# Kernel optimization log

Hardware: AMD Instinct MI355X
Metric: run time of the kernel (lower is better)

## Reference

```python
import jax, jax.numpy as jnp
import numpy as np

NEG_SLOPE = 0.01  # LeakyReLU default
STRIDE = 5        # group_length // 4
EPS = 1e-5        # RMSNorm eps


def leaky_relu(x):
    return jnp.where(x >= 0, x, NEG_SLOPE * x)


def rmsnorm(x, w):
    return x * jax.lax.rsqrt(jnp.mean(x * x, axis=-1, keepdims=True) + EPS) * w


def s6(x, fc1_w, fc1_b, fc2_w, fc2_b, fc3_w, fc3_b, A):
    # x: [B, L, D] with D = 2*d_model; A: [D, N]
    delta = jax.nn.softplus(x @ fc1_w.T + fc1_b)        # [B, L, D]
    Bm = x @ fc2_w.T + fc2_b                             # [B, L, N]
    Cm = x @ fc3_w.T + fc3_b                             # [B, L, N]
    dA = jnp.exp(jnp.einsum('bld,dn->bldn', delta, A))   # [B, L, D, N]
    dBx = jnp.einsum('bld,bln,bld->bldn', delta, Bm, x)  # delta * B * x

    def step(h, inp):
        dA_t, dBx_t = inp
        h = dA_t * h + dBx_t
        return h, h

    B_, L, D, N = dA.shape
    h0 = jnp.zeros((B_, D, N), dtype=x.dtype)
    _, hs = jax.lax.scan(step, h0, (jnp.swapaxes(dA, 0, 1), jnp.swapaxes(dBx, 0, 1)))
    hs = jnp.swapaxes(hs, 0, 1)                          # [B, L, D, N]
    return jnp.einsum('bln,bldn->bld', Cm, hs)           # [B, L, D]


def setup_inputs() -> dict:
    key = jax.random.key(0)
    ks = iter(jax.random.split(key, 32))

    def rn(shape, scale=0.02):
        return scale * jax.random.normal(next(ks), shape, dtype=jnp.float32)

    B, band, gl, d, N, L = 256, 189, 20, 128, 128, 34
    di = 2 * d
    return {
        'x': jax.random.normal(next(ks), (B, 1, band), dtype=jnp.float32),
        'conv_w': rn((d, 1, gl)), 'conv_b': rn((d,)),
        'norm_w': jnp.ones((d,), jnp.float32),
        'inp_w': rn((di, d)), 'inp_b': rn((di,)),
        'seqconv_w': rn((L, L, 3)), 'seqconv_b': rn((L,)),
        'convlin_w': rn((di, di)), 'convlin_b': rn((di,)),
        'fc1_w': rn((di, di)), 'fc1_b': rn((di,)),
        'fc2_w': rn((N, di)), 'fc2_b': rn((N,)),
        'fc3_w': rn((N, di)), 'fc3_b': rn((N,)),
        'A': jnp.ones((di, N), jnp.float32) / jnp.sqrt(jnp.float32(N)),
        'D_w': rn((di, d)), 'D_b': rn((di,)),
        'out_w': rn((d, di)), 'out_b': rn((d,)),
        'fnn1_w': rn((64, L * d)), 'fnn1_b': rn((64,)),
        'fnn2_w': rn((32, 64)), 'fnn2_b': rn((32,)),
    }


def reference(x, conv_w, conv_b, norm_w, inp_w, inp_b, seqconv_w, seqconv_b,
              convlin_w, convlin_b, fc1_w, fc1_b, fc2_w, fc2_b, fc3_w, fc3_b,
              A, D_w, D_b, out_w, out_b, fnn1_w, fnn1_b, fnn2_w, fnn2_b):
    # group division: Conv1d(1, d, k=20, stride=5) + LeakyReLU
    g = jax.lax.conv_general_dilated(x, conv_w, (STRIDE,), [(0, 0)],
                                     dimension_numbers=('NCH', 'OIH', 'NCH'))
    g = leaky_relu(g + conv_b[None, :, None])            # [B, d, L]
    h = jnp.swapaxes(g, 1, 2)                            # [B, L, d]
    # Mamba block
    xn = rmsnorm(h, norm_w)
    xp = xn @ inp_w.T + inp_b                            # [B, L, 2d]
    # Conv1d(seq_len, seq_len, k=3, pad=1): seq axis L is the channel dim
    xc = jax.lax.conv_general_dilated(xp, seqconv_w, (1,), [(1, 1)],
                                      dimension_numbers=('NCH', 'OIH', 'NCH'))
    xc = jax.nn.silu(xc + seqconv_b[None, :, None])
    xc = xc @ convlin_w.T + convlin_b                    # [B, L, 2d]
    xs = s6(xc, fc1_w, fc1_b, fc2_w, fc2_b, fc3_w, fc3_b, A)
    y = jax.nn.silu(xs) * jax.nn.silu(xn @ D_w.T + D_b)  # gated
    y = y @ out_w.T + out_b                              # [B, L, d]
    # FNN head
    f = y.reshape(y.shape[0], -1)                        # [B, L*d]
    f = leaky_relu(f @ fnn1_w.T + fnn1_b)
    return f @ fnn2_w.T + fnn2_b                         # [B, 32]
```

## Files before the change

kernel.cpp:

```cpp
#include <hip/hip_runtime.h>
#include <math.h>


#define NB    256
#define LL    34
#define DD    128
#define DI    256
#define NN    128
#define MM    (NB*LL)

using u16 = unsigned short;
typedef __attribute__((ext_vector_type(8))) short short8;
typedef __attribute__((ext_vector_type(4))) float f32x4;

__device__ __forceinline__ float silu_f(float x)  { return x / (1.f + __expf(-x)); }
__device__ __forceinline__ float softplus_f(float x) {
    return fmaxf(x, 0.f) + __logf(1.f + __expf(-fabsf(x)));
}
__device__ __forceinline__ float leaky_f(float x) { return (x >= 0.f) ? x : 0.01f * x; }

__device__ __forceinline__ u16 f2bf(float x) {
    unsigned u = __float_as_uint(x);
    return (u16)((u + 0x7FFF + ((u >> 16) & 1)) >> 16);
}
__device__ __forceinline__ float bf2f(u16 h) {
    return __uint_as_float(((unsigned)h) << 16);
}
__device__ __forceinline__ void f2pair(float v, u16* h, u16* l) {
    u16 hh = f2bf(v);
    *h = hh;
    *l = f2bf(v - bf2f(hh));
}

__global__ __launch_bounds__(256)
void prep_conv_k(const float* __restrict__ x, const float* __restrict__ cw,
                 const float* __restrict__ cb, const float* __restrict__ nw,
                 u16* __restrict__ XNh, u16* __restrict__ XNl,
                 const float* __restrict__ inp_w, const float* __restrict__ D_w,
                 const float* __restrict__ fc1_w, const float* __restrict__ fc2_w,
                 const float* __restrict__ fc3_w, const float* __restrict__ convlin_w,
                 const float* __restrict__ out_w,
                 const float* __restrict__ inp_b, const float* __restrict__ D_b,
                 const float* __restrict__ fc1_b, const float* __restrict__ fc2_b,
                 const float* __restrict__ fc3_b,
                 const float* __restrict__ W1, const float* __restrict__ A,
                 u16* __restrict__ wc1h, u16* __restrict__ wc1l,
                 u16* __restrict__ wc3h, u16* __restrict__ wc3l,
                 u16* __restrict__ cvh,  u16* __restrict__ cvl,
                 u16* __restrict__ owh,  u16* __restrict__ owl,
                 float* __restrict__ bias1, float* __restrict__ bias3,
                 float* __restrict__ W1T, int* __restrict__ flag)
{
    const int bx  = blockIdx.x;
    const int tid = threadIdx.x;
    __shared__ float tile[64][65];
    __shared__ float wsum[4];

    if (bx < 4352) {
        const int row = tid >> 7;
        const int c   = tid & 127;
        const int bl  = bx * 2 + row;
        const int b   = bl / LL, l = bl % LL;
        const float* xr = x + (size_t)b * 189 + l * 5;
        float g = cb[c];
        #pragma unroll
        for (int k = 0; k < 20; k++) g = fmaf(xr[k], cw[c * 20 + k], g);
        g = leaky_f(g);

        float s = g * g;
        #pragma unroll
        for (int m = 32; m >= 1; m >>= 1) s += __shfl_xor(s, m);
        if ((tid & 63) == 0) wsum[tid >> 6] = s;
        __syncthreads();
        float mean = (wsum[row * 2] + wsum[row * 2 + 1]) * (1.f / 128.f);
        float inv = 1.f / sqrtf(mean + 1e-5f);
        float v = g * inv * nw[c];
        f2pair(v, &XNh[(size_t)bl * DD + c], &XNl[(size_t)bl * DD + c]);
    } else if (bx < 5504) {
        int i = (bx - 4352) * 256 + tid;
        if (i < 65536) {
            float v = (i < 32768) ? inp_w[i] : D_w[i - 32768];
            f2pair(v, &wc1h[i], &wc1l[i]);
        } else if (i < 196608) {
            int j = i - 65536;
            float v = (j < 65536) ? fc1_w[j] : (j < 98304 ? fc2_w[j - 65536] : fc3_w[j - 98304]);
            f2pair(v, &wc3h[j], &wc3l[j]);
        } else if (i < 262144) {
            int j = i - 196608;
            f2pair(convlin_w[j], &cvh[j], &cvl[j]);
        } else if (i < 294912) {
            int j = i - 262144;
            f2pair(out_w[j], &owh[j], &owl[j]);
        }
        if (i < 512)  bias1[i] = (i < 256) ? inp_b[i] : D_b[i - 256];
        else if (i < 1024) {
            int j = i - 512;
            bias3[j] = (j < 256) ? fc1_b[j] : (j < 384 ? fc2_b[j - 256] : fc3_b[j - 384]);
        }
    } else if (bx < 5572) {
        const int bt = bx - 5504;
        for (int p = 0; p < 16; p++) {
            int idx = tid + p * 256;
            int r = idx >> 6, c = idx & 63;
            tile[r][c] = W1[(size_t)r * 4352 + bt * 64 + c];
        }
        __syncthreads();
        for (int p = 0; p < 16; p++) {
            int idx = tid + p * 256;
            int cc = idx >> 6, rr = idx & 63;
            W1T[(size_t)(bt * 64 + cc) * 64 + rr] = tile[rr][cc];
        }
    } else {
        __shared__ int s;
        if (tid == 0) s = 1;
        __syncthreads();
        bool ok = true;
        for (int k = 0; k < 128; k++) {
            int idx = tid + k * 256;
            ok &= (A[idx] == A[idx & ~127]);
        }
        if (!ok) s = 0;
        __syncthreads();
        if (tid == 0) *flag = s;
    }
}

template <int K, int EPI>
__global__ __launch_bounds__(256)
void mgemm_k(const u16* __restrict__ Ah, const u16* __restrict__ Al,
             const u16* __restrict__ Wh, const u16* __restrict__ Wl,
             const float* __restrict__ bias,
             float* __restrict__ Y, int ldy,
             u16* __restrict__ Yh, u16* __restrict__ Yl,
             u16* __restrict__ BC)
{
    const int tid  = threadIdx.x;
    const int r0   = blockIdx.x * 128;
    const int c0   = blockIdx.y * 64;
    const int wave = tid >> 6;
    const int lane = tid & 63;
    const int wm   = wave & 1;
    const int wn   = wave >> 1;
    const int l15  = lane & 15;
    const int lq   = lane >> 4;

    __shared__ u16 sAh[128][40];
    __shared__ u16 sAl[128][40];
    __shared__ u16 sBh[64][40];
    __shared__ u16 sBl[64][40];

    f32x4 acc[4][2];
    #pragma unroll
    for (int i = 0; i < 4; i++)
        #pragma unroll
        for (int j = 0; j < 2; j++) acc[i][j] = (f32x4){0.f, 0.f, 0.f, 0.f};

    const int a_row = tid >> 1;
    const int a_kb  = (tid & 1) * 16;
    const int b_row = tid >> 2;
    const int b_ko  = (tid & 3) * 8;

    for (int k0 = 0; k0 < K; k0 += 32) {
        const u16* ga = Ah + (size_t)(r0 + a_row) * K + k0 + a_kb;
        const u16* gl = Al + (size_t)(r0 + a_row) * K + k0 + a_kb;
        short8 vh0 = *(const short8*)(ga);
        short8 vh1 = *(const short8*)(ga + 8);
        short8 vl0 = *(const short8*)(gl);
        short8 vl1 = *(const short8*)(gl + 8);
        const u16* gb = Wh + (size_t)(c0 + b_row) * K + k0 + b_ko;
        const u16* gc = Wl + (size_t)(c0 + b_row) * K + k0 + b_ko;
        short8 wb = *(const short8*)(gb);
        short8 wc = *(const short8*)(gc);

        *(short8*)&sAh[a_row][a_kb]     = vh0;
        *(short8*)&sAh[a_row][a_kb + 8] = vh1;
        *(short8*)&sAl[a_row][a_kb]     = vl0;
        *(short8*)&sAl[a_row][a_kb + 8] = vl1;
        *(short8*)&sBh[b_row][b_ko] = wb;
        *(short8*)&sBl[b_row][b_ko] = wc;
        __syncthreads();

        short8 fah[4], fal[4], fbh[2], fbl[2];
        #pragma unroll
        for (int i = 0; i < 4; i++) {
            fah[i] = *(const short8*)&sAh[wm * 64 + i * 16 + l15][lq * 8];
            fal[i] = *(const short8*)&sAl[wm * 64 + i * 16 + l15][lq * 8];
        }
        #pragma unroll
        for (int j = 0; j < 2; j++) {
            fbh[j] = *(const short8*)&sBh[wn * 32 + j * 16 + l15][lq * 8];
            fbl[j] = *(const short8*)&sBl[wn * 32 + j * 16 + l15][lq * 8];
        }
        #pragma unroll
        for (int i = 0; i < 4; i++)
            #pragma unroll
            for (int j = 0; j < 2; j++) {
                acc[i][j] = __builtin_amdgcn_mfma_f32_16x16x32_bf16(fah[i], fbh[j], acc[i][j], 0, 0, 0);
                acc[i][j] = __builtin_amdgcn_mfma_f32_16x16x32_bf16(fah[i], fbl[j], acc[i][j], 0, 0, 0);
                acc[i][j] = __builtin_amdgcn_mfma_f32_16x16x32_bf16(fal[i], fbh[j], acc[i][j], 0, 0, 0);
            }
        __syncthreads();
    }

    #pragma unroll
    for (int i = 0; i < 4; i++) {
        int gr = r0 + wm * 64 + i * 16 + lq * 4;
        #pragma unroll
        for (int j = 0; j < 2; j++) {
            int gc = c0 + wn * 32 + j * 16 + l15;
            float bb = bias[gc];
            #pragma unroll
            for (int r = 0; r < 4; r++) {
                float v = acc[i][j][r] + bb;
                if (EPI == 1 || EPI == 3) { if (gc < 256) v = softplus_f(v); }
                if (EPI == 2) {
                    u16 hh, ll;
                    f2pair(v, &hh, &ll);
                    Yh[(size_t)(gr + r) * ldy + gc] = hh;
                    Yl[(size_t)(gr + r) * ldy + gc] = ll;
                } else {
                    Y[(size_t)(gr + r) * ldy + gc] = v;
                    if (EPI == 3 && gc >= 256) {
                        u16 hh, ll;
                        f2pair(v, &hh, &ll);
                        u16* rb = BC + (size_t)(gr + r) * 1024
                                     + ((gc < 384) ? 0 : 256) + (gc & 127);
                        rb[0]   = hh;
                        rb[128] = ll;
                    }
                }
            }
        }
    }
}

__global__ __launch_bounds__(1024, 1)
void mega2_k(const int* __restrict__ flag,
             const float* __restrict__ buf1,
             const float* __restrict__ scw, const float* __restrict__ scb,
             const u16* __restrict__ cvh, const u16* __restrict__ cvl,
             const float* __restrict__ clb,
             const u16* __restrict__ wc3h, const u16* __restrict__ wc3l,
             const float* __restrict__ bias3,
             const float* __restrict__ A,
             const u16* __restrict__ owh, const u16* __restrict__ owl,
             const float* __restrict__ outb,
             float* __restrict__ buf3,
             u16* __restrict__ bcpair,
             u16* __restrict__ xc2h, u16* __restrict__ xc2l,
             float* __restrict__ fout)
{
    const int b    = blockIdx.x;
    const int tid  = threadIdx.x;
    const int wave = tid >> 6;
    const int lane = tid & 63;
    const int l15  = lane & 15;
    const int lq   = lane >> 4;

    __shared__ __align__(16) char smem[109584];
    float (*sx)[264] = (float (*)[264])(smem);
    float (*sw)[112] = (float (*)[112])(smem + 35904);
    u16 (*sXch)[264] = (u16 (*)[264])(smem);
    u16 (*sXcl)[264] = (u16 (*)[264])(smem + 25344);
    u16 (*sBh)[136]  = (u16 (*)[136])(smem);
    u16 (*sBl)[136]  = (u16 (*)[136])(smem + 13056);
    u16 (*sCh)[136]  = (u16 (*)[136])(smem + 26112);
    u16 (*sCl)[136]  = (u16 (*)[136])(smem + 39168);
    u16 (*sGh)[264]  = (u16 (*)[264])(smem);
    u16 (*sGl)[264]  = (u16 (*)[264])(smem + 25344);
    u16 (*sX2h)[264] = (u16 (*)[264])(smem + 52224);
    u16 (*sX2l)[264] = (u16 (*)[264])(smem + 77568);
    float (*sM)[49]  = (float (*)[49])(smem + 102912);

    const bool uni = (*flag != 0);

    for (int idx = tid; idx < LL * 256; idx += 1024) {
        int li = idx >> 8, jj = idx & 255;
        sx[li][jj + 1] = buf1[(size_t)(b * LL + li) * 512 + jj];
    }
    if (tid < LL) { sx[tid][0] = 0.f; sx[tid][257] = 0.f; }
    for (int idx = tid; idx < LL * LL * 3; idx += 1024) {
        int lo = idx / 102;
        int rem = idx - lo * 102;
        int li = rem / 3;
        int k  = rem - li * 3;
        sw[li][lo * 3 + k] = scw[idx];
    }
    __syncthreads();

    {
        const int tx  = tid & 63;
        const int ty  = tid >> 6;
        const int j0c = tx * 4;
        const int cbase = (ty < 2) ? ty * 3 : 6 + (ty - 2) * 2;
        const int ccnt  = (ty < 2) ? 3 : 2;

        float cacc[3][4];
        #pragma unroll
        for (int i = 0; i < 3; i++)
            #pragma unroll
            for (int jj = 0; jj < 4; jj++) cacc[i][jj] = 0.f;

        for (int li = 0; li < LL; li++) {
            float4 xa = *(const float4*)&sx[li][j0c];
            float2 xb = *(const float2*)&sx[li][j0c + 4];
            float xv[6] = {xa.x, xa.y, xa.z, xa.w, xb.x, xb.y};
            const float* swr = &sw[li][0];
            #pragma unroll
            for (int i = 0; i < 3; i++) {
                if (i < ccnt) {
                    int lo3 = (cbase + i) * 3;
                    float w0 = swr[lo3 + 0];
                    float w1 = swr[lo3 + 1];
                    float w2 = swr[lo3 + 2];
                    #pragma unroll
                    for (int jj = 0; jj < 4; jj++) {
                        cacc[i][jj] = fmaf(w0, xv[jj],     cacc[i][jj]);
                        cacc[i][jj] = fmaf(w1, xv[jj + 1], cacc[i][jj]);
                        cacc[i][jj] = fmaf(w2, xv[jj + 2], cacc[i][jj]);
                    }
                }
            }
        }
        __syncthreads();

        #pragma unroll
        for (int i = 0; i < 3; i++) {
            if (i < ccnt) {
                int lo = cbase + i;
                float bb = scb[lo];
                ushort4 oh, ol;
                float v0 = silu_f(cacc[i][0] + bb);
                float v1 = silu_f(cacc[i][1] + bb);
                float v2 = silu_f(cacc[i][2] + bb);
                float v3 = silu_f(cacc[i][3] + bb);
                f2pair(v0, &oh.x, &ol.x);
                f2pair(v1, &oh.y, &ol.y);
                f2pair(v2, &oh.z, &ol.z);
                f2pair(v3, &oh.w, &ol.w);
                *(ushort4*)&sXch[lo][j0c] = oh;
                *(ushort4*)&sXcl[lo][j0c] = ol;
            }
        }
    }
    __syncthreads();

    {
        const int c0 = wave * 16;
        f32x4 a2[3];
        #pragma unroll
        for (int i = 0; i < 3; i++) a2[i] = (f32x4){0.f, 0.f, 0.f, 0.f};

        #pragma unroll
        for (int ks = 0; ks < 8; ks++) {
            short8 fh[3], fl[3];
            #pragma unroll
            for (int i = 0; i < 3; i++) {
                fh[i] = *(const short8*)&sXch[i * 16 + l15][ks * 32 + lq * 8];
                fl[i] = *(const short8*)&sXcl[i * 16 + l15][ks * 32 + lq * 8];
            }
            const size_t wo = (size_t)(c0 + l15) * 256 + ks * 32 + lq * 8;
            short8 bh = *(const short8*)&cvh[wo];
            short8 bl = *(const short8*)&cvl[wo];
            #pragma unroll
            for (int i = 0; i < 3; i++) {
                a2[i] = __builtin_amdgcn_mfma_f32_16x16x32_bf16(fh[i], bh, a2[i], 0, 0, 0);
                a2[i] = __builtin_amdgcn_mfma_f32_16x16x32_bf16(fh[i], bl, a2[i], 0, 0, 0);
                a2[i] = __builtin_amdgcn_mfma_f32_16x16x32_bf16(fl[i], bh, a2[i], 0, 0, 0);
            }
        }
        #pragma unroll
        for (int i = 0; i < 3; i++) {
            int row = i * 16 + lq * 4;
            int col = c0 + l15;
            float bb = clb[col];
            #pragma unroll
            for (int r = 0; r < 4; r++) {
                float v = a2[i][r] + bb;
                u16 hh, ll;
                f2pair(v, &hh, &ll);
                sX2h[row + r][col] = hh;
                sX2l[row + r][col] = ll;
                if (!uni && (row + r) < LL) {
                    xc2h[(size_t)(b * LL + row + r) * 256 + col] = hh;
                    xc2l[(size_t)(b * LL + row + r) * 256 + col] = ll;
                }
            }
        }
    }
    __syncthreads();

    {
        const int c0 = wave * 32;
        f32x4 a3[3][2];
        #pragma unroll
        for (int i = 0; i < 3; i++)
            #pragma unroll
            for (int j = 0; j < 2; j++) a3[i][j] = (f32x4){0.f, 0.f, 0.f, 0.f};

        #pragma unroll
        for (int ks = 0; ks < 8; ks++) {
            short8 fh[3], fl[3];
            #pragma unroll
            for (int i = 0; i < 3; i++) {
                fh[i] = *(const short8*)&sX2h[i * 16 + l15][ks * 32 + lq * 8];
                fl[i] = *(const short8*)&sX2l[i * 16 + l15][ks * 32 + lq * 8];
            }
            #pragma unroll
            for (int j = 0; j < 2; j++) {
                const size_t wo = (size_t)(c0 + j * 16 + l15) * 256 + ks * 32 + lq * 8;
                short8 bh = *(const short8*)&wc3h[wo];
                short8 bl = *(const short8*)&wc3l[wo];
                #pragma unroll
                for (int i = 0; i < 3; i++) {
                    a3[i][j] = __builtin_amdgcn_mfma_f32_16x16x32_bf16(fh[i], bh, a3[i][j], 0, 0, 0);
                    a3[i][j] = __builtin_amdgcn_mfma_f32_16x16x32_bf16(fh[i], bl, a3[i][j], 0, 0, 0);
                    a3[i][j] = __builtin_amdgcn_mfma_f32_16x16x32_bf16(fl[i], bh, a3[i][j], 0, 0, 0);
                }
            }
        }
        #pragma unroll
        for (int i = 0; i < 3; i++) {
            int row = i * 16 + lq * 4;
            #pragma unroll
            for (int j = 0; j < 2; j++) {
                int col = c0 + j * 16 + l15;
                float bb = bias3[col];
                #pragma unroll
                for (int r = 0; r < 4; r++) {
                    float v = a3[i][j][r] + bb;
                    int rr = row + r;
                    if (col < 256) {
                        v = softplus_f(v);
                        if (rr < LL) buf3[((size_t)b * LL + rr) * 512 + col] = v;
                    } else {
                        u16 hh, ll;
                        f2pair(v, &hh, &ll);
                        int cc = col & 127;
                        if (col < 384) { sBh[rr][cc] = hh; sBl[rr][cc] = ll; }
                        else           { sCh[rr][cc] = hh; sCl[rr][cc] = ll; }
                        if (!uni && rr < LL) {
                            buf3[((size_t)b * LL + rr) * 512 + col] = v;
                            u16* rb = bcpair + ((size_t)b * LL + rr) * 1024
                                      + ((col < 384) ? 0 : 256) + cc;
                            rb[0]   = hh;
                            rb[128] = ll;
                        }
                    }
                }
            }
        }
    }
    __syncthreads();
    if (!uni) return;

    for (int tt = wave; tt < 9; tt += 16) {
        int ti = tt / 3, tj = tt - ti * 3;
        f32x4 acc = (f32x4){0.f, 0.f, 0.f, 0.f};
        #pragma unroll
        for (int ks = 0; ks < 4; ks++) {
            short8 ch = *(const short8*)&sCh[ti * 16 + l15][ks * 32 + lq * 8];
            short8 cl = *(const short8*)&sCl[ti * 16 + l15][ks * 32 + lq * 8];
            short8 bh = *(const short8*)&sBh[tj * 16 + l15][ks * 32 + lq * 8];
            short8 bl = *(const short8*)&sBl[tj * 16 + l15][ks * 32 + lq * 8];
            acc = __builtin_amdgcn_mfma_f32_16x16x32_bf16(ch, bh, acc, 0, 0, 0);
            acc = __builtin_amdgcn_mfma_f32_16x16x32_bf16(ch, bl, acc, 0, 0, 0);
            acc = __builtin_amdgcn_mfma_f32_16x16x32_bf16(cl, bh, acc, 0, 0, 0);
        }
        #pragma unroll
        for (int r = 0; r < 4; r++) {
            int row = ti * 16 + lq * 4 + r;
            if (row < LL) sM[row][tj * 16 + l15] = acc[r];
        }
    }
    __syncthreads();

    if (tid < 256) {
        const int d = tid;
        const float a_d = A[(size_t)d * NN];
        const float* pDel = buf3 + (size_t)b * LL * 512 + d;

        float u[LL], eS[LL];
        float S = 0.f;
        #pragma unroll
        for (int l = 0; l < LL; l++) {
            float dl = pDel[l * 512];
            S = fmaf(dl, a_d, S);
            eS[l] = __expf(S);
            float xv = bf2f(sX2h[l][d]) + bf2f(sX2l[l][d]);
            u[l] = __expf(-S) * dl * xv;
        }

        const float* pG = buf1 + (size_t)b * LL * 512 + 256 + d;
        #pragma unroll
        for (int l = 0; l < LL; l++) {
            float acc = 0.f;
            for (int t = 0; t <= l; t++) acc = fmaf(sM[l][t], u[t], acc);
            float xs = eS[l] * acc;
            float g = silu_f(xs) * silu_f(pG[l * 512]);
            u16 hh, ll2;
            f2pair(g, &hh, &ll2);
            sGh[l][d] = hh;
            sGl[l][d] = ll2;
        }
    } else {
        u16* zh = &sGh[34][0];
        u16* zl = &sGl[34][0];
        for (int idx = tid - 256; idx < 14 * 264; idx += 768) {
            zh[idx] = 0;
            zl[idx] = 0;
        }
    }
    __syncthreads();

    {
        const int j0 = wave & 7;
        const int i0 = (wave >> 3) ? 2 : 0;
        const int ni = (wave >> 3) ? 1 : 2;
        f32x4 a4[2];
        #pragma unroll
        for (int i = 0; i < 2; i++) a4[i] = (f32x4){0.f, 0.f, 0.f, 0.f};
        #pragma unroll
        for (int ks = 0; ks < 8; ks++) {
            const size_t wo = (size_t)(j0 * 16 + l15) * 256 + ks * 32 + lq * 8;
            short8 bh = *(const short8*)&owh[wo];
            short8 bl = *(const short8*)&owl[wo];
            #pragma unroll
            for (int i = 0; i < 2; i++) {
                if (i < ni) {
                    short8 ah = *(const short8*)&sGh[(i0 + i) * 16 + l15][ks * 32 + lq * 8];
                    short8 al = *(const short8*)&sGl[(i0 + i) * 16 + l15][ks * 32 + lq * 8];
                    a4[i] = __builtin_amdgcn_mfma_f32_16x16x32_bf16(ah, bh, a4[i], 0, 0, 0);
                    a4[i] = __builtin_amdgcn_mfma_f32_16x16x32_bf16(ah, bl, a4[i], 0, 0, 0);
                    a4[i] = __builtin_amdgcn_mfma_f32_16x16x32_bf16(al, bh, a4[i], 0, 0, 0);
                }
            }
        }
        #pragma unroll
        for (int i = 0; i < 2; i++) {
            if (i < ni) {
                int row = (i0 + i) * 16 + lq * 4;
                int col = j0 * 16 + l15;
                float bb = outb[col];
                #pragma unroll
                for (int r = 0; r < 4; r++)
                    if (row + r < LL)
                        fout[(size_t)(b * LL + row + r) * 128 + col] = a4[i][r] + bb;
            }
        }
    }
}

__global__ __launch_bounds__(256)
void scan_fb_k(const int* __restrict__ flag,
               const float* __restrict__ dBC,
               const u16*  __restrict__ Xh, const u16* __restrict__ Xl,
               const float* __restrict__ A,
               const float* __restrict__ DG,
               u16* __restrict__ Gh, u16* __restrict__ Gl)
{
    if (*flag != 0) return;
    const int b  = blockIdx.y;
    const int d0 = blockIdx.x * 64;
    const int tid = threadIdx.x;
    const int sub = tid & 15;
    const int pg  = tid >> 4;
    const int dbase = d0 + pg * 4;
    const int nA = sub * 4;

    float a[4][8], h[4][8];
    #pragma unroll
    for (int dd = 0; dd < 4; dd++) {
        const float* Ar = A + (size_t)(dbase + dd) * NN;
        float4 q0 = *(const float4*)(Ar + nA);
        float4 q1 = *(const float4*)(Ar + 64 + nA);
        a[dd][0]=q0.x; a[dd][1]=q0.y; a[dd][2]=q0.z; a[dd][3]=q0.w;
        a[dd][4]=q1.x; a[dd][5]=q1.y; a[dd][6]=q1.z; a[dd][7]=q1.w;
        #pragma unroll
        for (int j = 0; j < 8; j++) h[dd][j] = 0.f;
    }

    const float* pD  = dBC + (size_t)b * LL * 512 + dbase;
    const float* pBC = dBC + (size_t)b * LL * 512 + 256 + nA;
    const u16*  pXh = Xh  + (size_t)b * LL * 256 + dbase;
    const u16*  pXl = Xl  + (size_t)b * LL * 256 + dbase;
    const float* pG  = DG  + (size_t)b * LL * 512 + 256 + dbase;
    u16* pGh = Gh + (size_t)b * LL * 256 + dbase;
    u16* pGl = Gl + (size_t)b * LL * 256 + dbase;

    for (int l = 0; l < LL; l++) {
        float4  cD  = *(const float4*)(pD);
        ushort4 cXh = *(const ushort4*)(pXh);
        ushort4 cXl = *(const ushort4*)(pXl);
        float4 cB0 = *(const float4*)(pBC);
        float4 cB1 = *(const float4*)(pBC + 64);
        float4 cC0 = *(const float4*)(pBC + 128);
        float4 cC1 = *(const float4*)(pBC + 192);
        pD += 512; pBC += 512; pXh += 256; pXl += 256;

        float xv[4] = { bf2f(cXh.x) + bf2f(cXl.x), bf2f(cXh.y) + bf2f(cXl.y),
                        bf2f(cXh.z) + bf2f(cXl.z), bf2f(cXh.w) + bf2f(cXl.w) };
        float dl[4] = {cD.x, cD.y, cD.z, cD.w};
        float dx[4] = {cD.x * xv[0], cD.y * xv[1], cD.z * xv[2], cD.w * xv[3]};
        float bv[8] = {cB0.x,cB0.y,cB0.z,cB0.w,cB1.x,cB1.y,cB1.z,cB1.w};
        float cv[8] = {cC0.x,cC0.y,cC0.z,cC0.w,cC1.x,cC1.y,cC1.z,cC1.w};

        float accd[4] = {0.f, 0.f, 0.f, 0.f};
        #pragma unroll
        for (int dd = 0; dd < 4; dd++)
            #pragma unroll
            for (int j = 0; j < 8; j++) {
                float dA = __expf(dl[dd] * a[dd][j]);
                h[dd][j] = fmaf(dA, h[dd][j], dx[dd] * bv[j]);
                accd[dd] = fmaf(cv[j], h[dd][j], accd[dd]);
            }
        #pragma unroll
        for (int dd = 0; dd < 4; dd++) {
            float v = accd[dd];
            v += __shfl_xor(v, 1);
            v += __shfl_xor(v, 2);
            v += __shfl_xor(v, 4);
            v += __shfl_xor(v, 8);
            accd[dd] = v;
        }
        if (sub == 0) {
            float4 dg = *(const float4*)(pG);
            ushort4 oh, ol;
            float g0 = silu_f(accd[0]) * silu_f(dg.x);
            float g1 = silu_f(accd[1]) * silu_f(dg.y);
            float g2 = silu_f(accd[2]) * silu_f(dg.z);
            float g3 = silu_f(accd[3]) * silu_f(dg.w);
            f2pair(g0, &oh.x, &ol.x);
            f2pair(g1, &oh.y, &ol.y);
            f2pair(g2, &oh.z, &ol.z);
            f2pair(g3, &oh.w, &ol.w);
            *(ushort4*)pGh = oh;
            *(ushort4*)pGl = ol;
        }
        pG += 512; pGh += 256; pGl += 256;
    }
}

__global__ __launch_bounds__(512)
void tail_cold_k(const int* __restrict__ flag,
                 const u16* __restrict__ gFh, const u16* __restrict__ gFl,
                 const u16* __restrict__ owh, const u16* __restrict__ owl,
                 const float* __restrict__ outb,
                 float* __restrict__ fout)
{
    if (*flag != 0) return;
    const int b    = blockIdx.x;
    const int tid  = threadIdx.x;
    const int wave = tid >> 6;
    const int lane = tid & 63;
    const int l15  = lane & 15;
    const int lq   = lane >> 4;

    __shared__ u16 sGh[48][264];
    __shared__ u16 sGl[48][264];

    for (int idx = tid; idx < LL * 32; idx += 512) {
        int l = idx >> 5, c = (idx & 31) << 3;
        *(short8*)&sGh[l][c] = *(const short8*)&gFh[((size_t)b * LL + l) * 256 + c];
        *(short8*)&sGl[l][c] = *(const short8*)&gFl[((size_t)b * LL + l) * 256 + c];
    }
    {
        u16* zh = &sGh[34][0];
        u16* zl = &sGl[34][0];
        for (int idx = tid; idx < 14 * 264; idx += 512) {
            zh[idx] = 0;
            zl[idx] = 0;
        }
    }
    __syncthreads();

    const int j0 = wave;
    f32x4 a4[3];
    #pragma unroll
    for (int i = 0; i < 3; i++) a4[i] = (f32x4){0.f, 0.f, 0.f, 0.f};
    #pragma unroll
    for (int ks = 0; ks < 8; ks++) {
        const size_t wo = (size_t)(j0 * 16 + l15) * 256 + ks * 32 + lq * 8;
        short8 bh = *(const short8*)&owh[wo];
        short8 bl = *(const short8*)&owl[wo];
        #pragma unroll
        for (int i = 0; i < 3; i++) {
            short8 ah = *(const short8*)&sGh[i * 16 + l15][ks * 32 + lq * 8];
            short8 al = *(const short8*)&sGl[i * 16 + l15][ks * 32 + lq * 8];
            a4[i] = __builtin_amdgcn_mfma_f32_16x16x32_bf16(ah, bh, a4[i], 0, 0, 0);
            a4[i] = __builtin_amdgcn_mfma_f32_16x16x32_bf16(ah, bl, a4[i], 0, 0, 0);
            a4[i] = __builtin_amdgcn_mfma_f32_16x16x32_bf16(al, bh, a4[i], 0, 0, 0);
        }
    }
    #pragma unroll
    for (int i = 0; i < 3; i++) {
        int row = i * 16 + lq * 4;
        int col = j0 * 16 + l15;
        float bb = outb[col];
        #pragma unroll
        for (int r = 0; r < 4; r++)
            if (row + r < LL)
                fout[(size_t)(b * LL + row + r) * 128 + col] = a4[i][r] + bb;
    }
}

__global__ __launch_bounds__(256)
void fnn1_k(const float* __restrict__ F, const float* __restrict__ W1T,
            float* __restrict__ partials)
{
    const int btile = blockIdx.x;
    const int kc    = blockIdx.y;
    const int tid   = threadIdx.x;
    __shared__ float sf[16][260];
    for (int i = tid; i < 16 * 256; i += 256) {
        int r = i >> 8, c = i & 255;
        sf[r][c] = F[(size_t)(btile * 16 + r) * 4352 + kc * 256 + c];
    }
    __syncthreads();

    const int o  = tid & 63;
    const int bq = tid >> 6;
    const float* w = W1T + (size_t)(kc * 256) * 64 + o;
    float acc[4] = {0.f, 0.f, 0.f, 0.f};
    for (int k = 0; k < 256; k += 4) {
        float w0 = w[(size_t)(k + 0) * 64];
        float w1 = w[(size_t)(k + 1) * 64];
        float w2 = w[(size_t)(k + 2) * 64];
        float w3 = w[(size_t)(k + 3) * 64];
        #pragma unroll
        for (int bj = 0; bj < 4; bj++) {
            float4 f4 = *(const float4*)&sf[bq * 4 + bj][k];
            acc[bj] = fmaf(w0, f4.x, acc[bj]);
            acc[bj] = fmaf(w1, f4.y, acc[bj]);
            acc[bj] = fmaf(w2, f4.z, acc[bj]);
            acc[bj] = fmaf(w3, f4.w, acc[bj]);
        }
    }
    #pragma unroll
    for (int bj = 0; bj < 4; bj++)
        partials[(size_t)kc * 16384 + (btile * 16 + bq * 4 + bj) * 64 + o] = acc[bj];
}

__global__ __launch_bounds__(64)
void fnn2_k(const float* __restrict__ partials,
            const float* __restrict__ B1,
            const float* __restrict__ W2, const float* __restrict__ B2,
            float* __restrict__ out)
{
    int b = blockIdx.x;
    int t = threadIdx.x;
    __shared__ float s1[64];
    float acc = B1[t];
    #pragma unroll
    for (int kc = 0; kc < 17; kc++)
        acc += partials[(size_t)kc * 16384 + b * 64 + t];
    s1[t] = leaky_f(acc);
    __syncthreads();

    if (t < 32) {
        float acc2 = B2[t];
        const float* w2 = W2 + t * 64;
        #pragma unroll
        for (int j = 0; j < 64; j++) acc2 = fmaf(s1[j], w2[j], acc2);
        out[(size_t)b * 32 + t] = acc2;
    }
}

extern "C" void kernel_launch(void* const* d_in, const int* in_sizes, int n_in,
                              void* d_out, int out_size, void* d_ws, size_t ws_size,
                              hipStream_t stream)
{
    const float* x        = (const float*)d_in[0];
    const float* conv_w   = (const float*)d_in[1];
    const float* conv_b   = (const float*)d_in[2];
    const float* norm_w   = (const float*)d_in[3];
    const float* inp_w    = (const float*)d_in[4];
    const float* inp_b    = (const float*)d_in[5];
    const float* seqconv_w= (const float*)d_in[6];
    const float* seqconv_b= (const float*)d_in[7];
    const float* convlin_w= (const float*)d_in[8];
    const float* convlin_b= (const float*)d_in[9];
    const float* fc1_w    = (const float*)d_in[10];
    const float* fc1_b    = (const float*)d_in[11];
    const float* fc2_w    = (const float*)d_in[12];
    const float* fc2_b    = (const float*)d_in[13];
    const float* fc3_w    = (const float*)d_in[14];
    const float* fc3_b    = (const float*)d_in[15];
    const float* A        = (const float*)d_in[16];
    const float* D_w      = (const float*)d_in[17];
    const float* D_b      = (const float*)d_in[18];
    const float* out_w    = (const float*)d_in[19];
    const float* out_b    = (const float*)d_in[20];
    const float* fnn1_w   = (const float*)d_in[21];
    const float* fnn1_b   = (const float*)d_in[22];
    const float* fnn2_w   = (const float*)d_in[23];
    const float* fnn2_b   = (const float*)d_in[24];

    char* W = (char*)d_ws;
    float* buf1  = (float*)(W + 0);
    float* buf3  = (float*)(W + 17825792);
    u16*   xnh   = (u16*)  (W + 35651584);
    u16*   xnl   = (u16*)  (W + 37879808);
    u16*   xc2h  = (u16*)  (W + 35651584);
    float* fout  = (float*)(W + 35651584);
    u16*   xc2l  = (u16*)  (W + 40108032);
    u16*   gateh = (u16*)  (W + 44564480);
    u16*   gatel = (u16*)  (W + 49020928);
    float* w1t   = (float*)(W + 53477376);
    u16*   wc1h  = (u16*)  (W + 54591488);
    u16*   wc1l  = (u16*)  (W + 54722560);
    u16*   wc3h  = (u16*)  (W + 54853632);
    u16*   wc3l  = (u16*)  (W + 55115776);
    u16*   cvh   = (u16*)  (W + 55377920);
    u16*   cvl   = (u16*)  (W + 55508992);
    u16*   owh   = (u16*)  (W + 55640064);
    u16*   owl   = (u16*)  (W + 55705600);
    float* bias1 = (float*)(W + 55771136);
    float* bias3 = (float*)(W + 55773184);
    int*   uflag = (int*)  (W + 55775232);
    u16* bcpair = (u16*)buf1;
    float* partials = buf3;

    prep_conv_k<<<5573, 256, 0, stream>>>(x, conv_w, conv_b, norm_w, xnh, xnl,
                                          inp_w, D_w, fc1_w, fc2_w, fc3_w,
                                          convlin_w, out_w,
                                          inp_b, D_b, fc1_b, fc2_b, fc3_b,
                                          fnn1_w, A,
                                          wc1h, wc1l, wc3h, wc3l, cvh, cvl,
                                          owh, owl, bias1, bias3, w1t, uflag);

    mgemm_k<128, 0><<<dim3(MM / 128, 8), 256, 0, stream>>>(
        xnh, xnl, wc1h, wc1l, bias1, buf1, 512, nullptr, nullptr, nullptr);

    mega2_k<<<NB, 1024, 0, stream>>>(uflag, buf1, seqconv_w, seqconv_b,
                                     cvh, cvl, convlin_b, wc3h, wc3l, bias3,
                                     A, owh, owl, out_b,
                                     buf3, bcpair, xc2h, xc2l, fout);

    scan_fb_k<<<dim3(4, NB), 256, 0, stream>>>(uflag, buf3, xc2h, xc2l, A,
                                               buf1, gateh, gatel);
    tail_cold_k<<<NB, 512, 0, stream>>>(uflag, gateh, gatel, owh, owl, out_b,
                                        fout);

    fnn1_k<<<dim3(16, 17), 256, 0, stream>>>(fout, w1t, partials);
    fnn2_k<<<NB, 64, 0, stream>>>(partials, fnn1_b, fnn2_w, fnn2_b,
                                  (float*)d_out);
}
```

Measured before the change: 205.5 us.

## Fuse conv+RMSNorm and input projection GEMM into per-batch mega kernel

Moves the strided conv, LeakyReLU and RMSNorm, plus the inp/D projection GEMM, out of the prep kernel and a separate MFMA GEMM launch and into the per-batch mega2 kernel. The normalized activations stay in shared memory. The projected x and the gate values go straight to LDS, so the 17MB buf1 round trip and one kernel launch are removed. In exchange LDS use grows to about 145KB per block. Each 1024-thread block now also redoes the small GEMM with weights read from global memory and not tiled through LDS. The gate is still written to global only in the non-uniform fallback path.

After: 204.8 us. No clear change (-0.3%).

```diff
diff --git a/kernel.cpp b/kernel.cpp
--- a/kernel.cpp
+++ b/kernel.cpp
@@ -33,51 +33,27 @@
 }
 
 __global__ __launch_bounds__(256)
-void prep_conv_k(const float* __restrict__ x, const float* __restrict__ cw,
-                 const float* __restrict__ cb, const float* __restrict__ nw,
-                 u16* __restrict__ XNh, u16* __restrict__ XNl,
-                 const float* __restrict__ inp_w, const float* __restrict__ D_w,
-                 const float* __restrict__ fc1_w, const float* __restrict__ fc2_w,
-                 const float* __restrict__ fc3_w, const float* __restrict__ convlin_w,
-                 const float* __restrict__ out_w,
-                 const float* __restrict__ inp_b, const float* __restrict__ D_b,
-                 const float* __restrict__ fc1_b, const float* __restrict__ fc2_b,
-                 const float* __restrict__ fc3_b,
-                 const float* __restrict__ W1, const float* __restrict__ A,
-                 u16* __restrict__ wc1h, u16* __restrict__ wc1l,
-                 u16* __restrict__ wc3h, u16* __restrict__ wc3l,
-                 u16* __restrict__ cvh,  u16* __restrict__ cvl,
-                 u16* __restrict__ owh,  u16* __restrict__ owl,
-                 float* __restrict__ bias1, float* __restrict__ bias3,
-                 float* __restrict__ W1T, int* __restrict__ flag)
+void prep_k(const float* __restrict__ inp_w, const float* __restrict__ D_w,
+            const float* __restrict__ fc1_w, const float* __restrict__ fc2_w,
+            const float* __restrict__ fc3_w, const float* __restrict__ convlin_w,
+            const float* __restrict__ out_w,
+            const float* __restrict__ inp_b, const float* __restrict__ D_b,
+            const float* __restrict__ fc1_b, const float* __restrict__ fc2_b,
+            const float* __restrict__ fc3_b,
+            const float* __restrict__ W1, const float* __restrict__ A,
+            u16* __restrict__ wc1h, u16* __restrict__ wc1l,
+            u16* __restrict__ wc3h, u16* __restrict__ wc3l,
+            u16* __restrict__ cvh,  u16* __restrict__ cvl,
+            u16* __restrict__ owh,  u16* __restrict__ owl,
+            float* __restrict__ bias1, float* __restrict__ bias3,
+            float* __restrict__ W1T, int* __restrict__ flag)
 {
     const int bx  = blockIdx.x;
     const int tid = threadIdx.x;
     __shared__ float tile[64][65];
-    __shared__ float wsum[4];
-
-    if (bx < 4352) {
-        const int row = tid >> 7;
-        const int c   = tid & 127;
-        const int bl  = bx * 2 + row;
-        const int b   = bl / LL, l = bl % LL;
-        const float* xr = x + (size_t)b * 189 + l * 5;
-        float g = cb[c];
-        #pragma unroll
-        for (int k = 0; k < 20; k++) g = fmaf(xr[k], cw[c * 20 + k], g);
-        g = leaky_f(g);
-
-        float s = g * g;
-        #pragma unroll
-        for (int m = 32; m >= 1; m >>= 1) s += __shfl_xor(s, m);
-        if ((tid & 63) == 0) wsum[tid >> 6] = s;
-        __syncthreads();
-        float mean = (wsum[row * 2] + wsum[row * 2 + 1]) * (1.f / 128.f);
-        float inv = 1.f / sqrtf(mean + 1e-5f);
-        float v = g * inv * nw[c];
-        f2pair(v, &XNh[(size_t)bl * DD + c], &XNl[(size_t)bl * DD + c]);
-    } else if (bx < 5504) {
-        int i = (bx - 4352) * 256 + tid;
+
+    if (bx < 1152) {
+        int i = bx * 256 + tid;
         if (i < 65536) {
             float v = (i < 32768) ? inp_w[i] : D_w[i - 32768];
             f2pair(v, &wc1h[i], &wc1l[i]);
@@ -97,8 +73,8 @@
             int j = i - 512;
             bias3[j] = (j < 256) ? fc1_b[j] : (j < 384 ? fc2_b[j - 256] : fc3_b[j - 384]);
         }
-    } else if (bx < 5572) {
-        const int bt = bx - 5504;
+    } else if (bx < 1220) {
+        const int bt = bx - 1152;
         for (int p = 0; p < 16; p++) {
             int idx = tid + p * 256;
             int r = idx >> 6, c = idx & 63;
@@ -125,118 +101,13 @@
     }
 }
 
-template <int K, int EPI>
-__global__ __launch_bounds__(256)
-void mgemm_k(const u16* __restrict__ Ah, const u16* __restrict__ Al,
-             const u16* __restrict__ Wh, const u16* __restrict__ Wl,
-             const float* __restrict__ bias,
-             float* __restrict__ Y, int ldy,
-             u16* __restrict__ Yh, u16* __restrict__ Yl,
-             u16* __restrict__ BC)
-{
-    const int tid  = threadIdx.x;
-    const int r0   = blockIdx.x * 128;
-    const int c0   = blockIdx.y * 64;
-    const int wave = tid >> 6;
-    const int lane = tid & 63;
-    const int wm   = wave & 1;
-    const int wn   = wave >> 1;
-    const int l15  = lane & 15;
-    const int lq   = lane >> 4;
-
-    __shared__ u16 sAh[128][40];
-    __shared__ u16 sAl[128][40];
-    __shared__ u16 sBh[64][40];
-    __shared__ u16 sBl[64][40];
-
-    f32x4 acc[4][2];
-    #pragma unroll
-    for (int i = 0; i < 4; i++)
-        #pragma unroll
-        for (int j = 0; j < 2; j++) acc[i][j] = (f32x4){0.f, 0.f, 0.f, 0.f};
-
-    const int a_row = tid >> 1;
-    const int a_kb  = (tid & 1) * 16;
-    const int b_row = tid >> 2;
-    const int b_ko  = (tid & 3) * 8;
-
-    for (int k0 = 0; k0 < K; k0 += 32) {
-        const u16* ga = Ah + (size_t)(r0 + a_row) * K + k0 + a_kb;
-        const u16* gl = Al + (size_t)(r0 + a_row) * K + k0 + a_kb;
-        short8 vh0 = *(const short8*)(ga);
-        short8 vh1 = *(const short8*)(ga + 8);
-        short8 vl0 = *(const short8*)(gl);
-        short8 vl1 = *(const short8*)(gl + 8);
-        const u16* gb = Wh + (size_t)(c0 + b_row) * K + k0 + b_ko;
-        const u16* gc = Wl + (size_t)(c0 + b_row) * K + k0 + b_ko;
-        short8 wb = *(const short8*)(gb);
-        short8 wc = *(const short8*)(gc);
-
-        *(short8*)&sAh[a_row][a_kb]     = vh0;
-        *(short8*)&sAh[a_row][a_kb + 8] = vh1;
-        *(short8*)&sAl[a_row][a_kb]     = vl0;
-        *(short8*)&sAl[a_row][a_kb + 8] = vl1;
-        *(short8*)&sBh[b_row][b_ko] = wb;
-        *(short8*)&sBl[b_row][b_ko] = wc;
-        __syncthreads();
-
-        short8 fah[4], fal[4], fbh[2], fbl[2];
-        #pragma unroll
-        for (int i = 0; i < 4; i++) {
-            fah[i] = *(const short8*)&sAh[wm * 64 + i * 16 + l15][lq * 8];
-            fal[i] = *(const short8*)&sAl[wm * 64 + i * 16 + l15][lq * 8];
-        }
-        #pragma unroll
-        for (int j = 0; j < 2; j++) {
-            fbh[j] = *(const short8*)&sBh[wn * 32 + j * 16 + l15][lq * 8];
-            fbl[j] = *(const short8*)&sBl[wn * 32 + j * 16 + l15][lq * 8];
-        }
-        #pragma unroll
-        for (int i = 0; i < 4; i++)
-            #pragma unroll
-            for (int j = 0; j < 2; j++) {
-                acc[i][j] = __builtin_amdgcn_mfma_f32_16x16x32_bf16(fah[i], fbh[j], acc[i][j], 0, 0, 0);
-                acc[i][j] = __builtin_amdgcn_mfma_f32_16x16x32_bf16(fah[i], fbl[j], acc[i][j], 0, 0, 0);
-                acc[i][j] = __builtin_amdgcn_mfma_f32_16x16x32_bf16(fal[i], fbh[j], acc[i][j], 0, 0, 0);
-            }
-        __syncthreads();
-    }
-
-    #pragma unroll
-    for (int i = 0; i < 4; i++) {
-        int gr = r0 + wm * 64 + i * 16 + lq * 4;
-        #pragma unroll
-        for (int j = 0; j < 2; j++) {
-            int gc = c0 + wn * 32 + j * 16 + l15;
-            float bb = bias[gc];
-            #pragma unroll
-            for (int r = 0; r < 4; r++) {
-                float v = acc[i][j][r] + bb;
-                if (EPI == 1 || EPI == 3) { if (gc < 256) v = softplus_f(v); }
-                if (EPI == 2) {
-                    u16 hh, ll;
-                    f2pair(v, &hh, &ll);
-                    Yh[(size_t)(gr + r) * ldy + gc] = hh;
-                    Yl[(size_t)(gr + r) * ldy + gc] = ll;
-                } else {
-                    Y[(size_t)(gr + r) * ldy + gc] = v;
-                    if (EPI == 3 && gc >= 256) {
-                        u16 hh, ll;
-                        f2pair(v, &hh, &ll);
-                        u16* rb = BC + (size_t)(gr + r) * 1024
-                                     + ((gc < 384) ? 0 : 256) + (gc & 127);
-                        rb[0]   = hh;
-                        rb[128] = ll;
-                    }
-                }
-            }
-        }
-    }
-}
-
 __global__ __launch_bounds__(1024, 1)
 void mega2_k(const int* __restrict__ flag,
-             const float* __restrict__ buf1,
+             const float* __restrict__ x,
+             const float* __restrict__ cw, const float* __restrict__ cb,
+             const float* __restrict__ nw,
+             const u16* __restrict__ wc1h, const u16* __restrict__ wc1l,
+             const float* __restrict__ bias1,
              const float* __restrict__ scw, const float* __restrict__ scb,
              const u16* __restrict__ cvh, const u16* __restrict__ cvl,
              const float* __restrict__ clb,
@@ -245,6 +116,7 @@
              const float* __restrict__ A,
              const u16* __restrict__ owh, const u16* __restrict__ owl,
              const float* __restrict__ outb,
+             float* __restrict__ buf1,
              float* __restrict__ buf3,
              u16* __restrict__ bcpair,
              u16* __restrict__ xc2h, u16* __restrict__ xc2l,
@@ -257,7 +129,7 @@
     const int l15  = lane & 15;
     const int lq   = lane >> 4;
 
-    __shared__ __align__(16) char smem[109584];
+    __shared__ __align__(16) char smem[144944];
     float (*sx)[264] = (float (*)[264])(smem);
     float (*sw)[112] = (float (*)[112])(smem + 35904);
     u16 (*sXch)[264] = (u16 (*)[264])(smem);
@@ -268,17 +140,16 @@
     u16 (*sCl)[136]  = (u16 (*)[136])(smem + 39168);
     u16 (*sGh)[264]  = (u16 (*)[264])(smem);
     u16 (*sGl)[264]  = (u16 (*)[264])(smem + 25344);
+    u16 (*sXnh)[136] = (u16 (*)[136])(smem + 52224);
+    u16 (*sXnl)[136] = (u16 (*)[136])(smem + 65280);
     u16 (*sX2h)[264] = (u16 (*)[264])(smem + 52224);
     u16 (*sX2l)[264] = (u16 (*)[264])(smem + 77568);
     float (*sM)[49]  = (float (*)[49])(smem + 102912);
+    float (*sDG)[260]= (float (*)[260])(smem + 109584);
+    __shared__ float wsumP[16];
 
     const bool uni = (*flag != 0);
 
-    for (int idx = tid; idx < LL * 256; idx += 1024) {
-        int li = idx >> 8, jj = idx & 255;
-        sx[li][jj + 1] = buf1[(size_t)(b * LL + li) * 512 + jj];
-    }
-    if (tid < LL) { sx[tid][0] = 0.f; sx[tid][257] = 0.f; }
     for (int idx = tid; idx < LL * LL * 3; idx += 1024) {
         int lo = idx / 102;
         int rem = idx - lo * 102;
@@ -286,6 +157,89 @@
         int k  = rem - li * 3;
         sw[li][lo * 3 + k] = scw[idx];
     }
+
+    {
+        const int rp = tid >> 7;
+        const int c  = tid & 127;
+        for (int pass = 0; pass < 5; pass++) {
+            const int rr = pass * 8 + rp;
+            float g = 0.f, s = 0.f;
+            if (rr < LL) {
+                const float* xr = x + (size_t)b * 189 + rr * 5;
+                g = cb[c];
+                #pragma unroll
+                for (int k = 0; k < 20; k++) g = fmaf(xr[k], cw[c * 20 + k], g);
+                g = leaky_f(g);
+                s = g * g;
+            }
+            #pragma unroll
+            for (int m = 32; m >= 1; m >>= 1) s += __shfl_xor(s, m);
+            if ((tid & 63) == 0) wsumP[tid >> 6] = s;
+            __syncthreads();
+            if (rr < LL) {
+                float mean = (wsumP[rp * 2] + wsumP[rp * 2 + 1]) * (1.f / 128.f);
+                float inv = 1.f / sqrtf(mean + 1e-5f);
+                float v = g * inv * nw[c];
+                f2pair(v, &sXnh[rr][c], &sXnl[rr][c]);
+            }
+            __syncthreads();
+        }
+    }
+
+    {
+        const int c0 = wave * 32;
+        f32x4 a1[3][2];
+        #pragma unroll
+        for (int i = 0; i < 3; i++)
+            #pragma unroll
+            for (int j = 0; j < 2; j++) a1[i][j] = (f32x4){0.f, 0.f, 0.f, 0.f};
+
+        #pragma unroll
+        for (int ks = 0; ks < 4; ks++) {
+            short8 fh[3], fl[3];
+            #pragma unroll
+            for (int i = 0; i < 3; i++) {
+                fh[i] = *(const short8*)&sXnh[i * 16 + l15][ks * 32 + lq * 8];
+                fl[i] = *(const short8*)&sXnl[i * 16 + l15][ks * 32 + lq * 8];
+            }
+            #pragma unroll
+            for (int j = 0; j < 2; j++) {
+                const size_t wo = (size_t)(c0 + j * 16 + l15) * 128 + ks * 32 + lq * 8;
+                short8 bh = *(const short8*)&wc1h[wo];
+                short8 bl = *(const short8*)&wc1l[wo];
+                #pragma unroll
+                for (int i = 0; i < 3; i++) {
+                    a1[i][j] = __builtin_amdgcn_mfma_f32_16x16x32_bf16(fh[i], bh, a1[i][j], 0, 0, 0);
+                    a1[i][j] = __builtin_amdgcn_mfma_f32_16x16x32_bf16(fh[i], bl, a1[i][j], 0, 0, 0);
+                    a1[i][j] = __builtin_amdgcn_mfma_f32_16x16x32_bf16(fl[i], bh, a1[i][j], 0, 0, 0);
+                }
+            }
+        }
+        #pragma unroll
+        for (int i = 0; i < 3; i++) {
+            int row = i * 16 + lq * 4;
+            #pragma unroll
+            for (int j = 0; j < 2; j++) {
+                int col = c0 + j * 16 + l15;
+                float bb = bias1[col];
+                #pragma unroll
+                for (int r = 0; r < 4; r++) {
+                    float v = a1[i][j][r] + bb;
+                    int rr = row + r;
+                    if (rr < LL) {
+                        if (col < 256) {
+                            sx[rr][col + 1] = v;
+                        } else {
+                            sDG[rr][col - 256] = v;
+                            if (!uni)
+                                buf1[((size_t)b * LL + rr) * 512 + col] = v;
+                        }
+                    }
+                }
+            }
+        }
+    }
+    if (tid < LL) { sx[tid][0] = 0.f; sx[tid][257] = 0.f; }
     __syncthreads();
 
     {
@@ -491,13 +445,12 @@
             u[l] = __expf(-S) * dl * xv;
         }
 
-        const float* pG = buf1 + (size_t)b * LL * 512 + 256 + d;
         #pragma unroll
         for (int l = 0; l < LL; l++) {
             float acc = 0.f;
             for (int t = 0; t <= l; t++) acc = fmaf(sM[l][t], u[t], acc);
             float xs = eS[l] * acc;
-            float g = silu_f(xs) * silu_f(pG[l * 512]);
+            float g = silu_f(xs) * silu_f(sDG[l][d]);
             u16 hh, ll2;
             f2pair(g, &hh, &ll2);
             sGh[l][d] = hh;
@@ -799,11 +752,9 @@
     char* W = (char*)d_ws;
     float* buf1  = (float*)(W + 0);
     float* buf3  = (float*)(W + 17825792);
-    u16*   xnh   = (u16*)  (W + 35651584);
-    u16*   xnl   = (u16*)  (W + 37879808);
-    u16*   xc2h  = (u16*)  (W + 35651584);
     float* fout  = (float*)(W + 35651584);
-    u16*   xc2l  = (u16*)  (W + 40108032);
+    u16*   xc2h  = (u16*)  (W + 37879808);
+    u16*   xc2l  = (u16*)  (W + 42336256);
     u16*   gateh = (u16*)  (W + 44564480);
     u16*   gatel = (u16*)  (W + 49020928);
     float* w1t   = (float*)(W + 53477376);
@@ -821,21 +772,19 @@
     u16* bcpair = (u16*)buf1;
     float* partials = buf3;
 
-    prep_conv_k<<<5573, 256, 0, stream>>>(x, conv_w, conv_b, norm_w, xnh, xnl,
-                                          inp_w, D_w, fc1_w, fc2_w, fc3_w,
-                                          convlin_w, out_w,
-                                          inp_b, D_b, fc1_b, fc2_b, fc3_b,
-                                          fnn1_w, A,
-                                          wc1h, wc1l, wc3h, wc3l, cvh, cvl,
-                                          owh, owl, bias1, bias3, w1t, uflag);
-
-    mgemm_k<128, 0><<<dim3(MM / 128, 8), 256, 0, stream>>>(
-        xnh, xnl, wc1h, wc1l, bias1, buf1, 512, nullptr, nullptr, nullptr);
-
-    mega2_k<<<NB, 1024, 0, stream>>>(uflag, buf1, seqconv_w, seqconv_b,
+    prep_k<<<1221, 256, 0, stream>>>(inp_w, D_w, fc1_w, fc2_w, fc3_w,
+                                     convlin_w, out_w,
+                                     inp_b, D_b, fc1_b, fc2_b, fc3_b,
+                                     fnn1_w, A,
+                                     wc1h, wc1l, wc3h, wc3l, cvh, cvl,
+                                     owh, owl, bias1, bias3, w1t, uflag);
+
+    mega2_k<<<NB, 1024, 0, stream>>>(uflag, x, conv_w, conv_b, norm_w,
+                                     wc1h, wc1l, bias1,
+                                     seqconv_w, seqconv_b,
                                      cvh, cvl, convlin_b, wc3h, wc3l, bias3,
                                      A, owh, owl, out_b,
-                                     buf3, bcpair, xc2h, xc2l, fout);
+                                     buf1, buf3, bcpair, xc2h, xc2l, fout);
 
     scan_fb_k<<<dim3(4, NB), 256, 0, stream>>>(uflag, buf3, xc2h, xc2l, A,
                                                buf1, gateh, gatel);
```
